# Kernel tuning notes

Measured on AMD Instinct MI355X. Metric: run time of the kernel, lower is better.

Reference implementation:

```python
import jax, jax.numpy as jnp
import numpy as np

BITWIDTH = 8  # args.actBitwidth


def setup_inputs() -> dict:
    key = jax.random.key(0)
    k1, k2, k3 = jax.random.split(key, 3)
    x = jax.random.normal(k1, (32, 256, 56, 56), dtype=jnp.float32)
    # orthonormal-ish projection matrix (stand-in for PCA eigenvectors)
    u = jax.random.normal(k2, (256, 256), dtype=jnp.float32) / np.float32(np.sqrt(256.0))
    # positive per-channel clamp values
    clamp_val = jax.random.uniform(k3, (256,), dtype=jnp.float32) * 3.0 + 0.5
    return {"x": x, "u": u, "clamp_val": clamp_val}


def reference(x, u, clamp_val):
    N, C, H, W = x.shape
    x = jax.nn.relu(x)
    # [C, N*H*W] channel-major flatten (matches transpose(0,1).view(C,-1))
    im = jnp.transpose(x, (1, 0, 2, 3)).reshape(C, -1)
    mn = jnp.mean(im, axis=1, keepdims=True)
    im = im - mn
    # PCA projection
    p = u.T @ im  # [C, NHW]
    # per-channel symmetric clamp
    c = clamp_val[:, None]
    pq = jnp.clip(p, -c, c)
    # per-channel dynamic min/max uniform quantization (fused over channels)
    dmax = jnp.max(pq, axis=1, keepdims=True)
    dmin = jnp.min(pq, axis=1, keepdims=True)
    rng = dmax - dmin
    scale = (2.0 ** BITWIDTH - 1.0) / jnp.where(rng == 0, 1.0, rng)
    q = jnp.round((pq - dmin) * scale) / scale + dmin
    q = jnp.where(rng == 0, pq, q)
    # project back, re-center, add channel means
    out = u @ q
    out = out - jnp.mean(out, axis=1, keepdims=True) + mn
    return jnp.transpose(out.reshape(C, N, H, W), (1, 0, 2, 3))
```

## Files before the change

### kernel.cpp

```cpp
#include <hip/hip_runtime.h>
#include <stdint.h>

#define CH    256
#define HWsz  3136
#define NIMG  32
#define COLS  (NIMG * HWsz)
#define KB    32
#define TN    64

typedef float  f32x4  __attribute__((ext_vector_type(4)));
typedef __bf16 bf16x8 __attribute__((ext_vector_type(8)));

struct Stats {
  float mnsum[CH];
  float mn[CH];
  float poff[CH];
  unsigned dminK[CH];
  unsigned dmaxK[CH];
  float dminF[CH];
  float scaleF[CH];
  float invF[CH];
  float qsum[CH];
  float corr[CH];
  unsigned short u_bf[CH * CH];
  unsigned short uT_bf[CH * CH];
};

__device__ __forceinline__ unsigned short f2bf(float f) {
  union { float f; unsigned u; } v; v.f = f;
  unsigned r = v.u + 0x7fffu + ((v.u >> 16) & 1u);
  return (unsigned short)(r >> 16);
}
__device__ __forceinline__ float bf2f(unsigned short b) {
  union { unsigned u; float f; } v; v.u = ((unsigned)b) << 16;
  return v.f;
}
__device__ __forceinline__ unsigned fkey(float f) {
  unsigned u = __float_as_uint(f);
  return (u & 0x80000000u) ? ~u : (u | 0x80000000u);
}
__device__ __forceinline__ float funkey(unsigned k) {
  unsigned u = (k & 0x80000000u) ? (k & 0x7fffffffu) : ~k;
  return __uint_as_float(u);
}
__device__ __forceinline__ float dq(float v, float dmin, float sc, float inv) {
  return sc == 0.f ? v : fmaf(rintf((v - dmin) * sc), inv, dmin);
}

__global__ void k_init(const float* __restrict__ u, Stats* st) {
  int b = blockIdx.x, t = threadIdx.x;
  st->u_bf[b * CH + t]  = f2bf(u[b * CH + t]);
  st->uT_bf[b * CH + t] = f2bf(u[t * CH + b]);
  if (b == 0) {
    st->mnsum[t] = 0.f;
    st->qsum[t]  = 0.f;
    st->dminK[t] = 0xFFFFFFFFu;
    st->dmaxK[t] = 0u;
  }
}

__global__ __launch_bounds__(256) void k_relusum(const float* __restrict__ x, Stats* st) {
  int row = blockIdx.x;
  int c = row & (CH - 1);
  const float4* xr = (const float4*)(x + (size_t)row * HWsz);
  float s = 0.f;
  for (int i = threadIdx.x; i < HWsz / 4; i += 256) {
    float4 v = xr[i];
    s += fmaxf(v.x, 0.f) + fmaxf(v.y, 0.f) + fmaxf(v.z, 0.f) + fmaxf(v.w, 0.f);
  }
  for (int off = 32; off; off >>= 1) s += __shfl_down(s, off);
  __shared__ float w4[4];
  int lane = threadIdx.x & 63, wv = threadIdx.x >> 6;
  if (!lane) w4[wv] = s;
  __syncthreads();
  if (threadIdx.x == 0) atomicAdd(&st->mnsum[c], w4[0] + w4[1] + w4[2] + w4[3]);
}

__global__ void k_mn_poff(const float* __restrict__ u, Stats* st) {
  int t = threadIdx.x;
  __shared__ float smn[CH];
  float mn = st->mnsum[t] * (1.f / COLS);
  st->mn[t] = mn;
  smn[t] = mn;
  __syncthreads();
  float acc = 0.f;
  for (int c = 0; c < CH; ++c) acc += u[c * CH + t] * smn[c];
  st->poff[t] = acc;
}

__global__ void k_finalize(Stats* st) {
  int t = threadIdx.x;
  float dmin = funkey(st->dminK[t]);
  float dmax = funkey(st->dmaxK[t]);
  float rng = dmax - dmin;
  float sc = 0.f, inv = 0.f;
  if (rng != 0.f) { sc = 255.f / rng; inv = rng / 255.f; }
  st->dminF[t] = dmin; st->scaleF[t] = sc; st->invF[t] = inv;
}

__global__ void k_corr(const float* __restrict__ u, Stats* st) {
  int t = threadIdx.x;
  __shared__ float qm[CH];
  qm[t] = st->qsum[t] * (1.f / COLS);
  __syncthreads();
  float acc = 0.f;
  for (int r = 0; r < CH; ++r) acc += u[t * CH + r] * qm[r];
  st->corr[t] = st->mn[t] - acc;
}

template <bool PQ_BF16>
__global__ __launch_bounds__(256) void k_gemm1(const float* __restrict__ x,
                                               const float* __restrict__ clampv,
                                               Stats* __restrict__ st,
                                               void* __restrict__ pqbuf) {
  __shared__ __align__(16) unsigned ldsB[TN * 20];
  __shared__ float smin[CH];
  __shared__ float smax[CH];

  const int blk = blockIdx.x;
  const int n   = blk / (HWsz / TN);
  const int hw0 = (blk % (HWsz / TN)) * TN;
  const int t = threadIdx.x;
  const int lane = t & 63, wv = t >> 6;
  const int g = t & 15, cpair = t >> 4;
  const int sq = cpair >> 2, c2 = cpair & 3;
  const int q = lane >> 4, r15 = lane & 15;

  const float* xim = x + (size_t)n * CH * HWsz;
  const unsigned short* uT = st->uT_bf;

  f32x4 acc[4][4] = {};

  for (int kc = 0; kc < CH / KB; ++kc) {
    __syncthreads();
    {
      const float* r0 = xim + (size_t)(kc * KB + 2 * cpair) * HWsz + hw0 + 4 * g;
      const float4 va = *(const float4*)r0;
      const float4 vb = *(const float4*)(r0 + HWsz);
      const float a0[4] = {va.x, va.y, va.z, va.w};
      const float b0[4] = {vb.x, vb.y, vb.z, vb.w};
#pragma unroll
      for (int i = 0; i < 4; ++i) {
        const int j = 4 * g + i;
        const unsigned lo = f2bf(fmaxf(a0[i], 0.f));
        const unsigned hi = f2bf(fmaxf(b0[i], 0.f));
        ldsB[j * 20 + ((sq ^ ((j >> 3) & 3)) << 2) + c2] = lo | (hi << 16);
      }
    }
    __syncthreads();

    bf16x8 afr[4];
#pragma unroll
    for (int mt = 0; mt < 4; ++mt) {
      const int row = 64 * wv + 16 * mt + r15;
      afr[mt] = *(const bf16x8*)(uT + row * CH + kc * KB + q * 8);
    }
#pragma unroll
    for (int nt = 0; nt < 4; ++nt) {
      const int j = nt * 16 + r15;
      const bf16x8 bfr = *(const bf16x8*)((const unsigned short*)ldsB +
                                          (size_t)j * 40 + ((q ^ ((j >> 3) & 3)) << 3));
#pragma unroll
      for (int mt = 0; mt < 4; ++mt)
        acc[mt][nt] = __builtin_amdgcn_mfma_f32_16x16x32_bf16(afr[mt], bfr, acc[mt][nt], 0, 0, 0);
    }
  }

#pragma unroll
  for (int mt = 0; mt < 4; ++mt) {
#pragma unroll
    for (int reg = 0; reg < 4; ++reg) {
      const int row = 64 * wv + 16 * mt + 4 * q + reg;
      const float po = st->poff[row];
      const float cv = clampv[row];
      float mnv = 1e30f, mxv = -1e30f;
      const size_t obase = ((size_t)(n * CH + row)) * HWsz + hw0;
#pragma unroll
      for (int nt = 0; nt < 4; ++nt) {
        float v = acc[mt][nt][reg] - po;
        v = fminf(fmaxf(v, -cv), cv);
        mnv = fminf(mnv, v);
        mxv = fmaxf(mxv, v);
        const int jl = nt * 16 + r15;
        if (PQ_BF16) ((unsigned short*)pqbuf)[obase + jl] = f2bf(v);
        else         ((float*)pqbuf)[obase + jl] = v;
      }
#pragma unroll
      for (int m = 8; m; m >>= 1) {
        mnv = fminf(mnv, __shfl_xor(mnv, m));
        mxv = fmaxf(mxv, __shfl_xor(mxv, m));
      }
      if (r15 == 0) { smin[row] = mnv; smax[row] = mxv; }
    }
  }
  __syncthreads();
  atomicMin(&st->dminK[t], fkey(smin[t]));
  atomicMax(&st->dmaxK[t], fkey(smax[t]));
}

template <bool PQ_BF16>
__global__ __launch_bounds__(256) void k_qsum(const void* __restrict__ pqbuf,
                                              Stats* __restrict__ st) {
  const int blk = blockIdx.x;
  const int r = blk & (CH - 1);
  const float dmin = st->dminF[r], sc = st->scaleF[r], inv = st->invF[r];
  const size_t base = (size_t)blk * HWsz;
  float s = 0.f;
  if (PQ_BF16) {
    const ushort4* p = (const ushort4*)((const unsigned short*)pqbuf + base);
    for (int i = threadIdx.x; i < HWsz / 4; i += 256) {
      const ushort4 v = p[i];
      s += dq(bf2f(v.x), dmin, sc, inv) + dq(bf2f(v.y), dmin, sc, inv) +
           dq(bf2f(v.z), dmin, sc, inv) + dq(bf2f(v.w), dmin, sc, inv);
    }
  } else {
    const float4* p = (const float4*)((const float*)pqbuf + base);
    for (int i = threadIdx.x; i < HWsz / 4; i += 256) {
      const float4 v = p[i];
      s += dq(v.x, dmin, sc, inv) + dq(v.y, dmin, sc, inv) +
           dq(v.z, dmin, sc, inv) + dq(v.w, dmin, sc, inv);
    }
  }
  for (int off = 32; off; off >>= 1) s += __shfl_down(s, off);
  __shared__ float w4[4];
  int lane = threadIdx.x & 63, wv = threadIdx.x >> 6;
  if (!lane) w4[wv] = s;
  __syncthreads();
  if (threadIdx.x == 0) atomicAdd(&st->qsum[r], w4[0] + w4[1] + w4[2] + w4[3]);
}

template <bool PQ_BF16>
__global__ __launch_bounds__(256) void k_gemm2(const void* __restrict__ pqbuf,
                                               Stats* __restrict__ st,
                                               float* __restrict__ out) {
  __shared__ __align__(16) unsigned ldsB[TN * 20];

  const int blk = blockIdx.x;
  const int n   = blk / (HWsz / TN);
  const int hw0 = (blk % (HWsz / TN)) * TN;
  const int t = threadIdx.x;
  const int lane = t & 63, wv = t >> 6;
  const int g = t & 15, cpair = t >> 4;
  const int sq = cpair >> 2, c2 = cpair & 3;
  const int q = lane >> 4, r15 = lane & 15;

  const unsigned short* uA = st->u_bf;
  f32x4 acc[4][4] = {};

  for (int kc = 0; kc < CH / KB; ++kc) {
    __syncthreads();
    {
      const int R0 = kc * KB + 2 * cpair;
      const float d0 = st->dminF[R0],     s0 = st->scaleF[R0],     i0 = st->invF[R0];
      const float d1 = st->dminF[R0 + 1], s1 = st->scaleF[R0 + 1], i1 = st->invF[R0 + 1];
      const size_t b0 = ((size_t)(n * CH + R0)) * HWsz + hw0 + 4 * g;
      float a0[4], b1[4];
      if (PQ_BF16) {
        const ushort4 va = *(const ushort4*)((const unsigned short*)pqbuf + b0);
        const ushort4 vb = *(const ushort4*)((const unsigned short*)pqbuf + b0 + HWsz);
        a0[0] = bf2f(va.x); a0[1] = bf2f(va.y); a0[2] = bf2f(va.z); a0[3] = bf2f(va.w);
        b1[0] = bf2f(vb.x); b1[1] = bf2f(vb.y); b1[2] = bf2f(vb.z); b1[3] = bf2f(vb.w);
      } else {
        const float4 va = *(const float4*)((const float*)pqbuf + b0);
        const float4 vb = *(const float4*)((const float*)pqbuf + b0 + HWsz);
        a0[0] = va.x; a0[1] = va.y; a0[2] = va.z; a0[3] = va.w;
        b1[0] = vb.x; b1[1] = vb.y; b1[2] = vb.z; b1[3] = vb.w;
      }
#pragma unroll
      for (int i = 0; i < 4; ++i) {
        const int j = 4 * g + i;
        const unsigned lo = f2bf(dq(a0[i], d0, s0, i0));
        const unsigned hi = f2bf(dq(b1[i], d1, s1, i1));
        ldsB[j * 20 + ((sq ^ ((j >> 3) & 3)) << 2) + c2] = lo | (hi << 16);
      }
    }
    __syncthreads();

    bf16x8 afr[4];
#pragma unroll
    for (int mt = 0; mt < 4; ++mt) {
      const int row = 64 * wv + 16 * mt + r15;
      afr[mt] = *(const bf16x8*)(uA + row * CH + kc * KB + q * 8);
    }
#pragma unroll
    for (int nt = 0; nt < 4; ++nt) {
      const int j = nt * 16 + r15;
      const bf16x8 bfr = *(const bf16x8*)((const unsigned short*)ldsB +
                                          (size_t)j * 40 + ((q ^ ((j >> 3) & 3)) << 3));
#pragma unroll
      for (int mt = 0; mt < 4; ++mt)
        acc[mt][nt] = __builtin_amdgcn_mfma_f32_16x16x32_bf16(afr[mt], bfr, acc[mt][nt], 0, 0, 0);
    }
  }

#pragma unroll
  for (int mt = 0; mt < 4; ++mt) {
#pragma unroll
    for (int reg = 0; reg < 4; ++reg) {
      const int row = 64 * wv + 16 * mt + 4 * q + reg;
      const float cr = st->corr[row];
      const size_t obase = ((size_t)(n * CH + row)) * HWsz + hw0;
#pragma unroll
      for (int nt = 0; nt < 4; ++nt)
        out[obase + nt * 16 + r15] = acc[mt][nt][reg] + cr;
    }
  }
}

extern "C" void kernel_launch(void* const* d_in, const int* in_sizes, int n_in,
                              void* d_out, int out_size, void* d_ws, size_t ws_size,
                              hipStream_t stream) {
  const float* x  = (const float*)d_in[0];
  const float* u  = (const float*)d_in[1];
  const float* cv = (const float*)d_in[2];
  float* out = (float*)d_out;
  Stats* st = (Stats*)d_ws;

  const size_t pq_off = (sizeof(Stats) + 255) & ~(size_t)255;
  const bool bf = ws_size >= pq_off + (size_t)CH * COLS * 2;
  void* pq = bf ? (void*)((char*)d_ws + pq_off) : (void*)out;

  const int gemm_blocks = NIMG * (HWsz / TN);

  k_init<<<CH, CH, 0, stream>>>(u, st);
  k_relusum<<<NIMG * CH, 256, 0, stream>>>(x, st);
  k_mn_poff<<<1, CH, 0, stream>>>(u, st);
  if (bf) k_gemm1<true ><<<gemm_blocks, 256, 0, stream>>>(x, cv, st, pq);
  else    k_gemm1<false><<<gemm_blocks, 256, 0, stream>>>(x, cv, st, pq);
  k_finalize<<<1, CH, 0, stream>>>(st);
  if (bf) k_qsum<true ><<<NIMG * CH, 256, 0, stream>>>(pq, st);
  else    k_qsum<false><<<NIMG * CH, 256, 0, stream>>>(pq, st);
  k_corr<<<1, CH, 0, stream>>>(u, st);
  if (bf) k_gemm2<true ><<<gemm_blocks, 256, 0, stream>>>(pq, st, out);
  else    k_gemm2<false><<<gemm_blocks, 256, 0, stream>>>(pq, st, out);
}
```

Baseline: 337.4 us.

## Fuse relu-mean into GEMM1, defer mean/clamp, interleave bf16 pq, double-buffer LDS

Result: slower. 440.9 us (+30.7%).

```diff
diff --git a/kernel.cpp b/kernel.cpp
--- a/kernel.cpp
+++ b/kernel.cpp
@@ -15,6 +15,7 @@
   float mnsum[CH];
   float mn[CH];
   float poff[CH];
+  float clF[CH];
   unsigned dminK[CH];
   unsigned dmaxK[CH];
   float dminF[CH];
@@ -35,6 +36,9 @@
   union { unsigned u; float f; } v; v.u = ((unsigned)b) << 16;
   return v.f;
 }
+__device__ __forceinline__ unsigned pack_bf2(float a, float b) {
+  return (unsigned)f2bf(a) | ((unsigned)f2bf(b) << 16);
+}
 __device__ __forceinline__ unsigned fkey(float f) {
   unsigned u = __float_as_uint(f);
   return (u & 0x80000000u) ? ~u : (u | 0x80000000u);
@@ -42,6 +46,9 @@
 __device__ __forceinline__ float funkey(unsigned k) {
   unsigned u = (k & 0x80000000u) ? (k & 0x7fffffffu) : ~k;
   return __uint_as_float(u);
+}
+__device__ __forceinline__ float clampf(float v, float c) {
+  return fminf(fmaxf(v, -c), c);
 }
 __device__ __forceinline__ float dq(float v, float dmin, float sc, float inv) {
   return sc == 0.f ? v : fmaf(rintf((v - dmin) * sc), inv, dmin);
@@ -59,43 +66,215 @@
   }
 }
 
-__global__ __launch_bounds__(256) void k_relusum(const float* __restrict__ x, Stats* st) {
-  int row = blockIdx.x;
-  int c = row & (CH - 1);
-  const float4* xr = (const float4*)(x + (size_t)row * HWsz);
-  float s = 0.f;
-  for (int i = threadIdx.x; i < HWsz / 4; i += 256) {
-    float4 v = xr[i];
-    s += fmaxf(v.x, 0.f) + fmaxf(v.y, 0.f) + fmaxf(v.z, 0.f) + fmaxf(v.w, 0.f);
+template <bool ILV>
+__global__ __launch_bounds__(256) void k_gemm1(const float* __restrict__ x,
+                                               Stats* __restrict__ st,
+                                               void* __restrict__ pqv) {
+  __shared__ __align__(16) unsigned ldsB[2][TN * 20];
+  __shared__ float smin[CH];
+  __shared__ float smax[CH];
+
+  const int blk = blockIdx.x;
+  const int n   = blk / (HWsz / TN);
+  const int hw0 = (blk % (HWsz / TN)) * TN;
+  const int t = threadIdx.x;
+  const int lane = t & 63, wv = t >> 6;
+  const int g = t & 15, cpair = t >> 4;
+  const int sq = cpair >> 2, c2 = cpair & 3;
+  const int q = lane >> 4, r15 = lane & 15;
+
+  const float* xb = x + (size_t)n * CH * HWsz + hw0 + 4 * g;
+  const unsigned short* uT = st->uT_bf;
+
+  f32x4 acc[4][4] = {};
+  float4 va, vb;
+
+  auto ldrows = [&](int kc, float4& A, float4& B) {
+    const float* r0 = xb + (size_t)(kc * KB + 2 * cpair) * HWsz;
+    A = *(const float4*)r0;
+    B = *(const float4*)(r0 + HWsz);
+  };
+  auto stage = [&](int kc, int buf, float4 A, float4 B) {
+    float a[4] = {fmaxf(A.x, 0.f), fmaxf(A.y, 0.f), fmaxf(A.z, 0.f), fmaxf(A.w, 0.f)};
+    float b[4] = {fmaxf(B.x, 0.f), fmaxf(B.y, 0.f), fmaxf(B.z, 0.f), fmaxf(B.w, 0.f)};
+    float s0 = (a[0] + a[1]) + (a[2] + a[3]);
+    float s1 = (b[0] + b[1]) + (b[2] + b[3]);
+#pragma unroll
+    for (int m = 1; m < 16; m <<= 1) {
+      s0 += __shfl_xor(s0, m);
+      s1 += __shfl_xor(s1, m);
+    }
+    if (g == 0) {
+      const int R0 = kc * KB + 2 * cpair;
+      atomicAdd(&st->mnsum[R0], s0);
+      atomicAdd(&st->mnsum[R0 + 1], s1);
+    }
+#pragma unroll
+    for (int i = 0; i < 4; ++i) {
+      const int j = 4 * g + i;
+      ldsB[buf][j * 20 + (((sq ^ ((j >> 3) & 3)) << 2) | c2)] = pack_bf2(a[i], b[i]);
+    }
+  };
+
+  ldrows(0, va, vb);
+  stage(0, 0, va, vb);
+  if (CH / KB > 1) ldrows(1, va, vb);
+
+  for (int kc = 0; kc < CH / KB; ++kc) {
+    __syncthreads();
+    bf16x8 afr[4];
+#pragma unroll
+    for (int mt = 0; mt < 4; ++mt)
+      afr[mt] = *(const bf16x8*)(uT + (64 * wv + 16 * mt + r15) * CH + kc * KB + q * 8);
+    bf16x8 bfr[4];
+#pragma unroll
+    for (int nt = 0; nt < 4; ++nt) {
+      const int j = nt * 16 + r15;
+      bfr[nt] = *(const bf16x8*)((const unsigned short*)ldsB[kc & 1] +
+                                 (size_t)j * 40 + ((q ^ ((j >> 3) & 3)) << 3));
+    }
+    if (kc + 1 < CH / KB) stage(kc + 1, (kc + 1) & 1, va, vb);
+    if (kc + 2 < CH / KB) ldrows(kc + 2, va, vb);
+#pragma unroll
+    for (int nt = 0; nt < 4; ++nt)
+#pragma unroll
+      for (int mt = 0; mt < 4; ++mt)
+        acc[mt][nt] = __builtin_amdgcn_mfma_f32_16x16x32_bf16(afr[mt], bfr[nt], acc[mt][nt], 0, 0, 0);
   }
-  for (int off = 32; off; off >>= 1) s += __shfl_down(s, off);
-  __shared__ float w4[4];
-  int lane = threadIdx.x & 63, wv = threadIdx.x >> 6;
-  if (!lane) w4[wv] = s;
+
+#pragma unroll
+  for (int mt = 0; mt < 4; ++mt) {
+    if (ILV) {
+      unsigned short us[4][4];
+      float vr[4][4];
+#pragma unroll
+      for (int nt = 0; nt < 4; ++nt)
+#pragma unroll
+        for (int reg = 0; reg < 4; ++reg) {
+          us[nt][reg] = f2bf(acc[mt][nt][reg]);
+          vr[nt][reg] = bf2f(us[nt][reg]);
+        }
+#pragma unroll
+      for (int reg = 0; reg < 4; ++reg) {
+        float mnv = fminf(fminf(vr[0][reg], vr[1][reg]), fminf(vr[2][reg], vr[3][reg]));
+        float mxv = fmaxf(fmaxf(vr[0][reg], vr[1][reg]), fmaxf(vr[2][reg], vr[3][reg]));
+#pragma unroll
+        for (int m = 8; m; m >>= 1) {
+          mnv = fminf(mnv, __shfl_xor(mnv, m));
+          mxv = fmaxf(mxv, __shfl_xor(mxv, m));
+        }
+        if (r15 == 0) {
+          const int row = 64 * wv + 16 * mt + 4 * q + reg;
+          smin[row] = mnv; smax[row] = mxv;
+        }
+      }
+      unsigned* pq32 = (unsigned*)pqv;
+      const int kp0 = 32 * wv + 8 * mt + 2 * q;
+#pragma unroll
+      for (int nt = 0; nt < 4; ++nt) {
+        const size_t base = ((size_t)n * (CH / 2) + kp0) * HWsz + hw0 + nt * 16 + r15;
+        pq32[base]        = (unsigned)us[nt][0] | ((unsigned)us[nt][1] << 16);
+        pq32[base + HWsz] = (unsigned)us[nt][2] | ((unsigned)us[nt][3] << 16);
+      }
+    } else {
+      float* pqf = (float*)pqv;
+#pragma unroll
+      for (int reg = 0; reg < 4; ++reg) {
+        const int row = 64 * wv + 16 * mt + 4 * q + reg;
+        float mnv = 1e30f, mxv = -1e30f;
+        const size_t obase = ((size_t)(n * CH + row)) * HWsz + hw0;
+#pragma unroll
+        for (int nt = 0; nt < 4; ++nt) {
+          float v = acc[mt][nt][reg];
+          mnv = fminf(mnv, v); mxv = fmaxf(mxv, v);
+          pqf[obase + nt * 16 + r15] = v;
+        }
+#pragma unroll
+        for (int m = 8; m; m >>= 1) {
+          mnv = fminf(mnv, __shfl_xor(mnv, m));
+          mxv = fmaxf(mxv, __shfl_xor(mxv, m));
+        }
+        if (r15 == 0) { smin[row] = mnv; smax[row] = mxv; }
+      }
+    }
+  }
   __syncthreads();
-  if (threadIdx.x == 0) atomicAdd(&st->mnsum[c], w4[0] + w4[1] + w4[2] + w4[3]);
-}
-
-__global__ void k_mn_poff(const float* __restrict__ u, Stats* st) {
+  atomicMin(&st->dminK[t], fkey(smin[t]));
+  atomicMax(&st->dmaxK[t], fkey(smax[t]));
+}
+
+__global__ void k_finalize(const float* __restrict__ u,
+                           const float* __restrict__ clampv, Stats* st) {
   int t = threadIdx.x;
   __shared__ float smn[CH];
-  float mn = st->mnsum[t] * (1.f / COLS);
-  st->mn[t] = mn;
-  smn[t] = mn;
+  float mnv = st->mnsum[t] * (1.f / COLS);
+  st->mn[t] = mnv;
+  smn[t] = mnv;
   __syncthreads();
   float acc = 0.f;
   for (int c = 0; c < CH; ++c) acc += u[c * CH + t] * smn[c];
   st->poff[t] = acc;
-}
-
-__global__ void k_finalize(Stats* st) {
-  int t = threadIdx.x;
-  float dmin = funkey(st->dminK[t]);
-  float dmax = funkey(st->dmaxK[t]);
+  float cv = clampv[t];
+  st->clF[t] = cv;
+  float dmin = clampf(funkey(st->dminK[t]) - acc, cv);
+  float dmax = clampf(funkey(st->dmaxK[t]) - acc, cv);
   float rng = dmax - dmin;
-  float sc = 0.f, inv = 0.f;
-  if (rng != 0.f) { sc = 255.f / rng; inv = rng / 255.f; }
-  st->dminF[t] = dmin; st->scaleF[t] = sc; st->invF[t] = inv;
+  float sc = 0.f, iv = 0.f;
+  if (rng != 0.f) { sc = 255.f / rng; iv = rng / 255.f; }
+  st->dminF[t] = dmin; st->scaleF[t] = sc; st->invF[t] = iv;
+}
+
+template <bool ILV>
+__global__ __launch_bounds__(256) void k_qsum(const void* __restrict__ pqv,
+                                              Stats* __restrict__ st) {
+  __shared__ float w4a[4], w4b[4];
+  const int blk = blockIdx.x;
+  if (ILV) {
+    const int kp = blk & (CH / 2 - 1);
+    const int r0 = 2 * kp, r1 = r0 + 1;
+    const float p0 = st->poff[r0], c0 = st->clF[r0], d0 = st->dminF[r0],
+                sc0 = st->scaleF[r0], i0 = st->invF[r0];
+    const float p1 = st->poff[r1], c1 = st->clF[r1], d1 = st->dminF[r1],
+                sc1 = st->scaleF[r1], i1 = st->invF[r1];
+    const uint4* p = (const uint4*)((const unsigned*)pqv + (size_t)blk * HWsz);
+    float s0 = 0.f, s1 = 0.f;
+    for (int i = threadIdx.x; i < HWsz / 4; i += 256) {
+      const uint4 w = p[i];
+      const unsigned ws[4] = {w.x, w.y, w.z, w.w};
+#pragma unroll
+      for (int k = 0; k < 4; ++k) {
+        s0 += dq(clampf(bf2f((unsigned short)(ws[k] & 0xffffu)) - p0, c0), d0, sc0, i0);
+        s1 += dq(clampf(bf2f((unsigned short)(ws[k] >> 16)) - p1, c1), d1, sc1, i1);
+      }
+    }
+    for (int off = 32; off; off >>= 1) {
+      s0 += __shfl_down(s0, off);
+      s1 += __shfl_down(s1, off);
+    }
+    int lane = threadIdx.x & 63, wvi = threadIdx.x >> 6;
+    if (!lane) { w4a[wvi] = s0; w4b[wvi] = s1; }
+    __syncthreads();
+    if (threadIdx.x == 0) {
+      atomicAdd(&st->qsum[r0], (w4a[0] + w4a[1]) + (w4a[2] + w4a[3]));
+      atomicAdd(&st->qsum[r1], (w4b[0] + w4b[1]) + (w4b[2] + w4b[3]));
+    }
+  } else {
+    const int r = blk & (CH - 1);
+    const float pf = st->poff[r], cl = st->clF[r], dmin = st->dminF[r],
+                sc = st->scaleF[r], inv = st->invF[r];
+    const float4* p = (const float4*)((const float*)pqv + (size_t)blk * HWsz);
+    float s = 0.f;
+    for (int i = threadIdx.x; i < HWsz / 4; i += 256) {
+      const float4 v = p[i];
+      s += dq(clampf(v.x - pf, cl), dmin, sc, inv) + dq(clampf(v.y - pf, cl), dmin, sc, inv) +
+           dq(clampf(v.z - pf, cl), dmin, sc, inv) + dq(clampf(v.w - pf, cl), dmin, sc, inv);
+    }
+    for (int off = 32; off; off >>= 1) s += __shfl_down(s, off);
+    int lane = threadIdx.x & 63, wvi = threadIdx.x >> 6;
+    if (!lane) w4a[wvi] = s;
+    __syncthreads();
+    if (threadIdx.x == 0) atomicAdd(&st->qsum[r], (w4a[0] + w4a[1]) + (w4a[2] + w4a[3]));
+  }
 }
 
 __global__ void k_corr(const float* __restrict__ u, Stats* st) {
@@ -108,193 +287,95 @@
   st->corr[t] = st->mn[t] - acc;
 }
 
-template <bool PQ_BF16>
-__global__ __launch_bounds__(256) void k_gemm1(const float* __restrict__ x,
-                                               const float* __restrict__ clampv,
+template <bool ILV>
+__global__ __launch_bounds__(256) void k_gemm2(const void* __restrict__ pqv,
                                                Stats* __restrict__ st,
-                                               void* __restrict__ pqbuf) {
-  __shared__ __align__(16) unsigned ldsB[TN * 20];
-  __shared__ float smin[CH];
-  __shared__ float smax[CH];
+                                               float* __restrict__ out) {
+  __shared__ __align__(16) unsigned ldsB[2][TN * 20];
 
   const int blk = blockIdx.x;
   const int n   = blk / (HWsz / TN);
   const int hw0 = (blk % (HWsz / TN)) * TN;
   const int t = threadIdx.x;
   const int lane = t & 63, wv = t >> 6;
-  const int g = t & 15, cpair = t >> 4;
-  const int sq = cpair >> 2, c2 = cpair & 3;
+  const int g = t & 15;
+  const int kpl = t >> 4;
+  const int cpair = t >> 4;
+  const int sq = kpl >> 2, c2 = kpl & 3;
   const int q = lane >> 4, r15 = lane & 15;
 
-  const float* xim = x + (size_t)n * CH * HWsz;
-  const unsigned short* uT = st->uT_bf;
-
+  const unsigned short* uA = st->u_bf;
   f32x4 acc[4][4] = {};
+
+  uint4 wI;
+  float4 vaF, vbF;
+
+  auto ldrows = [&](int kc) {
+    if (ILV) {
+      wI = *(const uint4*)((const unsigned*)pqv +
+                           ((size_t)n * (CH / 2) + kc * 16 + kpl) * HWsz + hw0 + 4 * g);
+    } else {
+      const float* r0 = (const float*)pqv +
+                        ((size_t)(n * CH + kc * KB + 2 * cpair)) * HWsz + hw0 + 4 * g;
+      vaF = *(const float4*)r0;
+      vbF = *(const float4*)(r0 + HWsz);
+    }
+  };
+  auto stage = [&](int kc, int buf) {
+    const int R0 = ILV ? 2 * (kc * 16 + kpl) : kc * KB + 2 * cpair;
+    const float p0 = st->poff[R0],     c0 = st->clF[R0],     d0 = st->dminF[R0],
+                sc0 = st->scaleF[R0],  i0 = st->invF[R0];
+    const float p1 = st->poff[R0 + 1], c1 = st->clF[R0 + 1], d1 = st->dminF[R0 + 1],
+                sc1 = st->scaleF[R0 + 1], i1 = st->invF[R0 + 1];
+    float lo[4], hi[4];
+    if (ILV) {
+      const unsigned ws[4] = {wI.x, wI.y, wI.z, wI.w};
+#pragma unroll
+      for (int i = 0; i < 4; ++i) {
+        lo[i] = bf2f((unsigned short)(ws[i] & 0xffffu));
+        hi[i] = bf2f((unsigned short)(ws[i] >> 16));
+      }
+    } else {
+      lo[0] = vaF.x; lo[1] = vaF.y; lo[2] = vaF.z; lo[3] = vaF.w;
+      hi[0] = vbF.x; hi[1] = vbF.y; hi[2] = vbF.z; hi[3] = vbF.w;
+    }
+#pragma unroll
+    for (int i = 0; i < 4; ++i) {
+      const float v0 = dq(clampf(lo[i] - p0, c0), d0, sc0, i0);
+      const float v1 = dq(clampf(hi[i] - p1, c1), d1, sc1, i1);
+      const int j = 4 * g + i;
+      ldsB[buf][j * 20 + (((sq ^ ((j >> 3) & 3)) << 2) | c2)] = pack_bf2(v0, v1);
+    }
+  };
+
+  ldrows(0);
+  stage(0, 0);
+  if (CH / KB > 1) ldrows(1);
 
   for (int kc = 0; kc < CH / KB; ++kc) {
     __syncthreads();
-    {
-      const float* r0 = xim + (size_t)(kc * KB + 2 * cpair) * HWsz + hw0 + 4 * g;
-      const float4 va = *(const float4*)r0;
-      const float4 vb = *(const float4*)(r0 + HWsz);
-      const float a0[4] = {va.x, va.y, va.z, va.w};
-      const float b0[4] = {vb.x, vb.y, vb.z, vb.w};
-#pragma unroll
-      for (int i = 0; i < 4; ++i) {
-        const int j = 4 * g + i;
-        const unsigned lo = f2bf(fmaxf(a0[i], 0.f));
-        const unsigned hi = f2bf(fmaxf(b0[i], 0.f));
-        ldsB[j * 20 + ((sq ^ ((j >> 3) & 3)) << 2) + c2] = lo | (hi << 16);
-      }
-    }
-    __syncthreads();
-
     bf16x8 afr[4];
 #pragma unroll
-    for (int mt = 0; mt < 4; ++mt) {
-      const int row = 64 * wv + 16 * mt + r15;
-      afr[mt] = *(const bf16x8*)(uT + row * CH + kc * KB + q * 8);
-    }
+    for (int mt = 0; mt < 4; ++mt)
+      afr[mt] = *(const bf16x8*)(uA + (64 * wv + 16 * mt + r15) * CH + kc * KB + q * 8);
+    bf16x8 bfr[4];
 #pragma unroll
     for (int nt = 0; nt < 4; ++nt) {
       const int j = nt * 16 + r15;
-      const bf16x8 bfr = *(const bf16x8*)((const unsigned short*)ldsB +
-                                          (size_t)j * 40 + ((q ^ ((j >> 3) & 3)) << 3));
+      bfr[nt] = *(const bf16x8*)((const unsigned short*)ldsB[kc & 1] +
+                                 (size_t)j * 40 + ((q ^ ((j >> 3) & 3)) << 3));
+    }
+    if (kc + 1 < CH / KB) stage(kc + 1, (kc + 1) & 1);
+    if (kc + 2 < CH / KB) ldrows(kc + 2);
+#pragma unroll
+    for (int nt = 0; nt < 4; ++nt)
 #pragma unroll
       for (int mt = 0; mt < 4; ++mt)
-        acc[mt][nt] = __builtin_amdgcn_mfma_f32_16x16x32_bf16(afr[mt], bfr, acc[mt][nt], 0, 0, 0);
-    }
+        acc[mt][nt] = __builtin_amdgcn_mfma_f32_16x16x32_bf16(afr[mt], bfr[nt], acc[mt][nt], 0, 0, 0);
   }
 
 #pragma unroll
-  for (int mt = 0; mt < 4; ++mt) {
-#pragma unroll
-    for (int reg = 0; reg < 4; ++reg) {
-      const int row = 64 * wv + 16 * mt + 4 * q + reg;
-      const float po = st->poff[row];
-      const float cv = clampv[row];
-      float mnv = 1e30f, mxv = -1e30f;
-      const size_t obase = ((size_t)(n * CH + row)) * HWsz + hw0;
-#pragma unroll
-      for (int nt = 0; nt < 4; ++nt) {
-        float v = acc[mt][nt][reg] - po;
-        v = fminf(fmaxf(v, -cv), cv);
-        mnv = fminf(mnv, v);
-        mxv = fmaxf(mxv, v);
-        const int jl = nt * 16 + r15;
-        if (PQ_BF16) ((unsigned short*)pqbuf)[obase + jl] = f2bf(v);
-        else         ((float*)pqbuf)[obase + jl] = v;
-      }
-#pragma unroll
-      for (int m = 8; m; m >>= 1) {
-        mnv = fminf(mnv, __shfl_xor(mnv, m));
-        mxv = fmaxf(mxv, __shfl_xor(mxv, m));
-      }
-      if (r15 == 0) { smin[row] = mnv; smax[row] = mxv; }
-    }
-  }
-  __syncthreads();
-  atomicMin(&st->dminK[t], fkey(smin[t]));
-  atomicMax(&st->dmaxK[t], fkey(smax[t]));
-}
-
-template <bool PQ_BF16>
-__global__ __launch_bounds__(256) void k_qsum(const void* __restrict__ pqbuf,
-                                              Stats* __restrict__ st) {
-  const int blk = blockIdx.x;
-  const int r = blk & (CH - 1);
-  const float dmin = st->dminF[r], sc = st->scaleF[r], inv = st->invF[r];
-  const size_t base = (size_t)blk * HWsz;
-  float s = 0.f;
-  if (PQ_BF16) {
-    const ushort4* p = (const ushort4*)((const unsigned short*)pqbuf + base);
-    for (int i = threadIdx.x; i < HWsz / 4; i += 256) {
-      const ushort4 v = p[i];
-      s += dq(bf2f(v.x), dmin, sc, inv) + dq(bf2f(v.y), dmin, sc, inv) +
-           dq(bf2f(v.z), dmin, sc, inv) + dq(bf2f(v.w), dmin, sc, inv);
-    }
-  } else {
-    const float4* p = (const float4*)((const float*)pqbuf + base);
-    for (int i = threadIdx.x; i < HWsz / 4; i += 256) {
-      const float4 v = p[i];
-      s += dq(v.x, dmin, sc, inv) + dq(v.y, dmin, sc, inv) +
-           dq(v.z, dmin, sc, inv) + dq(v.w, dmin, sc, inv);
-    }
-  }
-  for (int off = 32; off; off >>= 1) s += __shfl_down(s, off);
-  __shared__ float w4[4];
-  int lane = threadIdx.x & 63, wv = threadIdx.x >> 6;
-  if (!lane) w4[wv] = s;
-  __syncthreads();
-  if (threadIdx.x == 0) atomicAdd(&st->qsum[r], w4[0] + w4[1] + w4[2] + w4[3]);
-}
-
-template <bool PQ_BF16>
-__global__ __launch_bounds__(256) void k_gemm2(const void* __restrict__ pqbuf,
-                                               Stats* __restrict__ st,
-                                               float* __restrict__ out) {
-  __shared__ __align__(16) unsigned ldsB[TN * 20];
-
-  const int blk = blockIdx.x;
-  const int n   = blk / (HWsz / TN);
-  const int hw0 = (blk % (HWsz / TN)) * TN;
-  const int t = threadIdx.x;
-  const int lane = t & 63, wv = t >> 6;
-  const int g = t & 15, cpair = t >> 4;
-  const int sq = cpair >> 2, c2 = cpair & 3;
-  const int q = lane >> 4, r15 = lane & 15;
-
-  const unsigned short* uA = st->u_bf;
-  f32x4 acc[4][4] = {};
-
-  for (int kc = 0; kc < CH / KB; ++kc) {
-    __syncthreads();
-    {
-      const int R0 = kc * KB + 2 * cpair;
-      const float d0 = st->dminF[R0],     s0 = st->scaleF[R0],     i0 = st->invF[R0];
-      const float d1 = st->dminF[R0 + 1], s1 = st->scaleF[R0 + 1], i1 = st->invF[R0 + 1];
-      const size_t b0 = ((size_t)(n * CH + R0)) * HWsz + hw0 + 4 * g;
-      float a0[4], b1[4];
-      if (PQ_BF16) {
-        const ushort4 va = *(const ushort4*)((const unsigned short*)pqbuf + b0);
-        const ushort4 vb = *(const ushort4*)((const unsigned short*)pqbuf + b0 + HWsz);
-        a0[0] = bf2f(va.x); a0[1] = bf2f(va.y); a0[2] = bf2f(va.z); a0[3] = bf2f(va.w);
-        b1[0] = bf2f(vb.x); b1[1] = bf2f(vb.y); b1[2] = bf2f(vb.z); b1[3] = bf2f(vb.w);
-      } else {
-        const float4 va = *(const float4*)((const float*)pqbuf + b0);
-        const float4 vb = *(const float4*)((const float*)pqbuf + b0 + HWsz);
-        a0[0] = va.x; a0[1] = va.y; a0[2] = va.z; a0[3] = va.w;
-        b1[0] = vb.x; b1[1] = vb.y; b1[2] = vb.z; b1[3] = vb.w;
-      }
-#pragma unroll
-      for (int i = 0; i < 4; ++i) {
-        const int j = 4 * g + i;
-        const unsigned lo = f2bf(dq(a0[i], d0, s0, i0));
-        const unsigned hi = f2bf(dq(b1[i], d1, s1, i1));
-        ldsB[j * 20 + ((sq ^ ((j >> 3) & 3)) << 2) + c2] = lo | (hi << 16);
-      }
-    }
-    __syncthreads();
-
-    bf16x8 afr[4];
-#pragma unroll
-    for (int mt = 0; mt < 4; ++mt) {
-      const int row = 64 * wv + 16 * mt + r15;
-      afr[mt] = *(const bf16x8*)(uA + row * CH + kc * KB + q * 8);
-    }
-#pragma unroll
-    for (int nt = 0; nt < 4; ++nt) {
-      const int j = nt * 16 + r15;
-      const bf16x8 bfr = *(const bf16x8*)((const unsigned short*)ldsB +
-                                          (size_t)j * 40 + ((q ^ ((j >> 3) & 3)) << 3));
-#pragma unroll
-      for (int mt = 0; mt < 4; ++mt)
-        acc[mt][nt] = __builtin_amdgcn_mfma_f32_16x16x32_bf16(afr[mt], bfr, acc[mt][nt], 0, 0, 0);
-    }
-  }
-
-#pragma unroll
-  for (int mt = 0; mt < 4; ++mt) {
+  for (int mt = 0; mt < 4; ++mt)
 #pragma unroll
     for (int reg = 0; reg < 4; ++reg) {
       const int row = 64 * wv + 16 * mt + 4 * q + reg;
@@ -304,7 +385,6 @@
       for (int nt = 0; nt < 4; ++nt)
         out[obase + nt * 16 + r15] = acc[mt][nt][reg] + cr;
     }
-  }
 }
 
 extern "C" void kernel_launch(void* const* d_in, const int* in_sizes, int n_in,
@@ -317,20 +397,18 @@
   Stats* st = (Stats*)d_ws;
 
   const size_t pq_off = (sizeof(Stats) + 255) & ~(size_t)255;
-  const bool bf = ws_size >= pq_off + (size_t)CH * COLS * 2;
-  void* pq = bf ? (void*)((char*)d_ws + pq_off) : (void*)out;
+  const bool ilv = ws_size >= pq_off + (size_t)NIMG * (CH / 2) * HWsz * 4;
+  void* pq = ilv ? (void*)((char*)d_ws + pq_off) : (void*)out;
 
   const int gemm_blocks = NIMG * (HWsz / TN);
 
   k_init<<<CH, CH, 0, stream>>>(u, st);
-  k_relusum<<<NIMG * CH, 256, 0, stream>>>(x, st);
-  k_mn_poff<<<1, CH, 0, stream>>>(u, st);
-  if (bf) k_gemm1<true ><<<gemm_blocks, 256, 0, stream>>>(x, cv, st, pq);
-  else    k_gemm1<false><<<gemm_blocks, 256, 0, stream>>>(x, cv, st, pq);
-  k_finalize<<<1, CH, 0, stream>>>(st);
-  if (bf) k_qsum<true ><<<NIMG * CH, 256, 0, stream>>>(pq, st);
-  else    k_qsum<false><<<NIMG * CH, 256, 0, stream>>>(pq, st);
+  if (ilv) k_gemm1<true ><<<gemm_blocks, 256, 0, stream>>>(x, st, pq);
+  else     k_gemm1<false><<<gemm_blocks, 256, 0, stream>>>(x, st, pq);
+  k_finalize<<<1, CH, 0, stream>>>(u, cv, st);
+  if (ilv) k_qsum<true ><<<NIMG * (CH / 2), 256, 0, stream>>>(pq, st);
+  else     k_qsum<false><<<NIMG * CH, 256, 0, stream>>>(pq, st);
   k_corr<<<1, CH, 0, stream>>>(u, st);
-  if (bf) k_gemm2<true ><<<gemm_blocks, 256, 0, stream>>>(pq, st, out);
-  else    k_gemm2<false><<<gemm_blocks, 256, 0, stream>>>(pq, st, out);
-}
+  if (ilv) k_gemm2<true ><<<gemm_blocks, 256, 0, stream>>>(pq, st, out);
+  else     k_gemm2<false><<<gemm_blocks, 256, 0, stream>>>(pq, st, out);
+}
```
